# Kernel optimization log

Hardware: AMD Instinct MI355X
Metric: run time of the kernel (lower is better)

Reference implementation:

```python
import jax, jax.numpy as jnp
import numpy as np

N, D, E, H = 50000, 64, 800000, 64
LAMB = 0.8
EPS_COS = 1e-8
EPS_NORM = 1e-12


def _segment_mean(msgs, rows, n):
    # scatter_mean: sum messages per destination row, divide by in-count
    s = jax.ops.segment_sum(msgs, rows, num_segments=n)
    cnt = jax.ops.segment_sum(jnp.ones((msgs.shape[0],), msgs.dtype), rows, num_segments=n)
    return s / jnp.maximum(cnt, 1.0)[:, None]


def _l2_normalize(x):
    # F.normalize(p=2, dim=-1)
    n = jnp.linalg.norm(x, axis=-1, keepdims=True)
    return x / jnp.maximum(n, EPS_NORM)


def _base_agg(x, edges, W, b):
    row, col = edges[0], edges[1]
    agg = _segment_mean(x[col], row, x.shape[0])          # [N, D]
    out = jnp.concatenate([agg, x], axis=1) @ W + b       # [N, H]
    return _l2_normalize(out)


def _deep_agg(x1, x2, pos_edges, neg_edges, W, b):
    rp, cp = pos_edges[0], pos_edges[1]
    rn, cn = neg_edges[0], neg_edges[1]
    out1 = _segment_mean(x1[cp], rp, x1.shape[0])
    out2 = _segment_mean(x2[cn], rn, x2.shape[0])
    out = jnp.concatenate([out1, out2, x1], axis=1) @ W + b
    return _l2_normalize(out)


def _xavier(key, shape):
    fan_in, fan_out = shape
    std = np.sqrt(2.0 / (fan_in + fan_out))
    return jax.random.normal(key, shape, dtype=jnp.float32) * std


def setup_inputs() -> dict:
    key = jax.random.key(0)
    ks = jax.random.split(key, 12)
    X = jax.random.normal(ks[0], (N, D), dtype=jnp.float32)
    positive_edges = jax.random.randint(ks[1], (2, E), 0, N, dtype=jnp.int64)
    negative_edges = jax.random.randint(ks[2], (2, E), 0, N, dtype=jnp.int64)
    comm = jax.random.randint(ks[3], (N,), 0, 3, dtype=jnp.int64)
    return {
        "X": X,
        "pos_base_W": _xavier(ks[4], (2 * D, H)),
        "pos_base_b": jnp.zeros((H,), jnp.float32),
        "neg_base_W": _xavier(ks[5], (2 * D, H)),
        "neg_base_b": jnp.zeros((H,), jnp.float32),
        "pos_deep_W": _xavier(ks[6], (3 * H, H)),
        "pos_deep_b": jnp.zeros((H,), jnp.float32),
        "neg_deep_W": _xavier(ks[7], (3 * H, H)),
        "neg_deep_b": jnp.zeros((H,), jnp.float32),
        "reg_W": _xavier(ks[8], (2 * H, 3)),
        "reg_b": jnp.zeros((3,), jnp.float32),
        "positive_edges": positive_edges,
        "negative_edges": negative_edges,
        "comm": comm,
    }


def _cosine_sim(a, b):
    na = jnp.maximum(jnp.linalg.norm(a, axis=1), EPS_COS)
    nb = jnp.maximum(jnp.linalg.norm(b, axis=1), EPS_COS)
    return jnp.sum(a * b, axis=1) / (na * nb)


def reference(X, pos_base_W, pos_base_b, neg_base_W, neg_base_b,
              pos_deep_W, pos_deep_b, neg_deep_W, neg_deep_b,
              reg_W, reg_b, positive_edges, negative_edges, comm):
    # layer 0 (base aggregators) + tanh
    h_pos = jnp.tanh(_base_agg(X, positive_edges, pos_base_W, pos_base_b))
    h_neg = jnp.tanh(_base_agg(X, negative_edges, neg_base_W, neg_base_b))
    # layer 1 (deep aggregators, balance theory cross-wiring) + tanh
    h_pos2 = jnp.tanh(_deep_agg(h_pos, h_neg, positive_edges, negative_edges, pos_deep_W, pos_deep_b))
    h_neg2 = jnp.tanh(_deep_agg(h_neg, h_pos, positive_edges, negative_edges, neg_deep_W, neg_deep_b))
    z = jnp.concatenate([h_pos2, h_neg2], axis=1)          # [N, 2H]

    # nll community loss
    logits = z @ reg_W + reg_b                              # [N, 3]
    logp = jax.nn.log_softmax(logits, axis=1)
    clarify = jnp.argmax(logp, axis=1)                      # predicted classes (int)
    reg_loss = -jnp.mean(jnp.take_along_axis(logp, comm[:, None], axis=1))

    # positive similarity loss: penalize similar embeddings across predicted communities
    ip, jp = positive_edges[0], positive_edges[1]
    cos_p = _cosine_sim(z[ip], z[jp])
    sim1 = jnp.mean(jnp.where(clarify[ip] != clarify[jp], jnp.maximum(cos_p, 0.0), 0.0))

    # negative similarity loss: penalize dissimilar embeddings within predicted community
    in_, jn = negative_edges[0], negative_edges[1]
    cos_n = _cosine_sim(z[in_], z[jn])
    sim2 = jnp.mean(jnp.where(clarify[in_] == clarify[jn], -jnp.minimum(cos_n, 0.0), 0.0))

    loss = LAMB * reg_loss + (1.0 - LAMB) * (sim1 + sim2)
    return loss, z, clarify
```

## Files before the change

kernel.cpp:

```cpp
#include <hip/hip_runtime.h>
#include <hip/hip_bf16.h>
#include <math.h>

#define DFEAT 64

typedef unsigned int u32;
typedef unsigned short u16;

__device__ inline float bflo(u32 u) { return __uint_as_float(u << 16); }
__device__ inline float bfhi(u32 u) { return __uint_as_float(u & 0xffff0000u); }

__global__ void count_edges_k(const int* __restrict__ rows, int E, int* __restrict__ cnt) {
    int e = blockIdx.x * blockDim.x + threadIdx.x;
    if (e < E) atomicAdd(&cnt[rows[e]], 1);
}

__global__ __launch_bounds__(1024) void scan_k(const int* __restrict__ cnt_all, int n,
                                               int* __restrict__ offs_all, int* __restrict__ cur_all) {
    const int* cnt = cnt_all + (size_t)blockIdx.x * n;
    int* offs = offs_all + (size_t)blockIdx.x * (n + 1);
    int* cur  = cur_all  + (size_t)blockIdx.x * n;

    __shared__ int lsum[1024];
    int tid = threadIdx.x;
    int per = (n + 1023) / 1024;
    int start = tid * per;
    int s = 0;
    for (int j = 0; j < per; ++j) {
        int i = start + j;
        if (i < n) s += cnt[i];
    }
    lsum[tid] = s;
    __syncthreads();
    for (int off = 1; off < 1024; off <<= 1) {
        int v = (tid >= off) ? lsum[tid - off] : 0;
        __syncthreads();
        lsum[tid] += v;
        __syncthreads();
    }
    int running = lsum[tid] - s;
    for (int j = 0; j < per; ++j) {
        int i = start + j;
        if (i < n) {
            offs[i] = running;
            cur[i]  = running;
            running += cnt[i];
        }
    }
    if (tid == 1023) offs[n] = lsum[1023];
}

__global__ void fill_k(const int* __restrict__ rows, const int* __restrict__ cols, int E,
                       int* __restrict__ cur, int* __restrict__ col_list) {
    int e = blockIdx.x * blockDim.x + threadIdx.x;
    if (e < E) {
        int r = rows[e];
        int p = atomicAdd(&cur[r], 1);
        col_list[p] = cols[e];
    }
}

__global__ __launch_bounds__(256) void gatherX_k(
        const float* __restrict__ X,
        const int* __restrict__ offs_p, const int* __restrict__ col_p,
        const int* __restrict__ offs_n, const int* __restrict__ col_n,
        float* __restrict__ a1, float* __restrict__ a2, int n) {
    int y = blockIdx.y;
    const int* offs = y ? offs_n : offs_p;
    const int* cols = y ? col_n : col_p;
    float* o = y ? a2 : a1;
    int gid  = (blockIdx.x * blockDim.x + threadIdx.x) >> 6;
    int lane = threadIdx.x & 63;
    if (gid >= n) return;
    int beg = offs[gid], end = offs[gid + 1];
    float a = 0.f;
    int e = beg;
    for (; e + 7 < end; e += 8) {
        int c0 = cols[e],     c1 = cols[e + 1], c2 = cols[e + 2], c3 = cols[e + 3];
        int c4 = cols[e + 4], c5 = cols[e + 5], c6 = cols[e + 6], c7 = cols[e + 7];
        float v0 = X[(size_t)c0 * DFEAT + lane];
        float v1 = X[(size_t)c1 * DFEAT + lane];
        float v2 = X[(size_t)c2 * DFEAT + lane];
        float v3 = X[(size_t)c3 * DFEAT + lane];
        float v4 = X[(size_t)c4 * DFEAT + lane];
        float v5 = X[(size_t)c5 * DFEAT + lane];
        float v6 = X[(size_t)c6 * DFEAT + lane];
        float v7 = X[(size_t)c7 * DFEAT + lane];
        a += ((v0 + v1) + (v2 + v3)) + ((v4 + v5) + (v6 + v7));
    }
    for (; e + 3 < end; e += 4) {
        int c0 = cols[e], c1 = cols[e + 1], c2 = cols[e + 2], c3 = cols[e + 3];
        a += (X[(size_t)c0 * DFEAT + lane] + X[(size_t)c1 * DFEAT + lane])
           + (X[(size_t)c2 * DFEAT + lane] + X[(size_t)c3 * DFEAT + lane]);
    }
    for (; e < end; ++e) a += X[(size_t)cols[e] * DFEAT + lane];
    int deg = end - beg;
    o[(size_t)gid * DFEAT + lane] = a / (float)(deg > 1 ? deg : 1);
}

__global__ __launch_bounds__(256) void dual_gather_k(
        const float* __restrict__ hcat,
        const int* __restrict__ offs_p, const int* __restrict__ col_p,
        const int* __restrict__ offs_n, const int* __restrict__ col_n,
        float* __restrict__ a1, float* __restrict__ a2,
        float* __restrict__ z, int n) {
    int y = blockIdx.y;
    const int* offs = y ? offs_n : offs_p;
    const int* cols = y ? col_n : col_p;
    float* o1 = y ? (z + 64) : a1;  int os1 = y ? 128 : 64;
    float* o2 = y ? z        : a2;  int os2 = y ? 128 : 64;

    int gid  = (blockIdx.x * blockDim.x + threadIdx.x) >> 6;
    int lane = threadIdx.x & 63;
    if (gid >= n) return;
    int beg = offs[gid], end = offs[gid + 1];
    float sx = 0.f, sy = 0.f;
    int e = beg;
    for (; e + 7 < end; e += 8) {
        int c0 = cols[e],     c1 = cols[e + 1], c2 = cols[e + 2], c3 = cols[e + 3];
        int c4 = cols[e + 4], c5 = cols[e + 5], c6 = cols[e + 6], c7 = cols[e + 7];
        float2 v0 = *reinterpret_cast<const float2*>(hcat + (size_t)c0 * 128 + lane * 2);
        float2 v1 = *reinterpret_cast<const float2*>(hcat + (size_t)c1 * 128 + lane * 2);
        float2 v2 = *reinterpret_cast<const float2*>(hcat + (size_t)c2 * 128 + lane * 2);
        float2 v3 = *reinterpret_cast<const float2*>(hcat + (size_t)c3 * 128 + lane * 2);
        float2 v4 = *reinterpret_cast<const float2*>(hcat + (size_t)c4 * 128 + lane * 2);
        float2 v5 = *reinterpret_cast<const float2*>(hcat + (size_t)c5 * 128 + lane * 2);
        float2 v6 = *reinterpret_cast<const float2*>(hcat + (size_t)c6 * 128 + lane * 2);
        float2 v7 = *reinterpret_cast<const float2*>(hcat + (size_t)c7 * 128 + lane * 2);
        sx += ((v0.x + v1.x) + (v2.x + v3.x)) + ((v4.x + v5.x) + (v6.x + v7.x));
        sy += ((v0.y + v1.y) + (v2.y + v3.y)) + ((v4.y + v5.y) + (v6.y + v7.y));
    }
    for (; e + 3 < end; e += 4) {
        int c0 = cols[e], c1 = cols[e + 1], c2 = cols[e + 2], c3 = cols[e + 3];
        float2 v0 = *reinterpret_cast<const float2*>(hcat + (size_t)c0 * 128 + lane * 2);
        float2 v1 = *reinterpret_cast<const float2*>(hcat + (size_t)c1 * 128 + lane * 2);
        float2 v2 = *reinterpret_cast<const float2*>(hcat + (size_t)c2 * 128 + lane * 2);
        float2 v3 = *reinterpret_cast<const float2*>(hcat + (size_t)c3 * 128 + lane * 2);
        sx += (v0.x + v1.x) + (v2.x + v3.x);
        sy += (v0.y + v1.y) + (v2.y + v3.y);
    }
    for (; e < end; ++e) {
        float2 v = *reinterpret_cast<const float2*>(hcat + (size_t)cols[e] * 128 + lane * 2);
        sx += v.x; sy += v.y;
    }
    int deg = end - beg;
    float inv = 1.f / (float)(deg > 1 ? deg : 1);
    sx *= inv; sy *= inv;
    if (lane < 32) {
        o1[(size_t)gid * os1 + lane * 2]     = sx;
        o1[(size_t)gid * os1 + lane * 2 + 1] = sy;
    } else {
        o2[(size_t)gid * os2 + (lane - 32) * 2]     = sx;
        o2[(size_t)gid * os2 + (lane - 32) * 2 + 1] = sy;
    }
}

template<int K, bool HAS2>
__global__ __launch_bounds__(256) void fused_linear_k(
        const float* __restrict__ p1, int s1,
        const float* __restrict__ p2, int s2,
        const float* __restrict__ p3, int s3,
        const float* __restrict__ W, const float* __restrict__ b,
        float* __restrict__ out, int os) {
    __shared__ float Ws[K * 64];
    __shared__ float bs[64];
    __shared__ float cat[4][K];

    for (int idx = threadIdx.x; idx < K * 64; idx += 256) Ws[idx] = W[idx];
    if (threadIdx.x < 64) bs[threadIdx.x] = b[threadIdx.x];

    int wave = threadIdx.x >> 6;
    int lane = threadIdx.x & 63;
    int row  = blockIdx.x * 4 + wave;

    cat[wave][lane] = p1[(size_t)row * s1 + lane];
    if (HAS2) {
        cat[wave][64 + lane]  = p2[(size_t)row * s2 + lane];
        cat[wave][128 + lane] = p3[(size_t)row * s3 + lane];
    } else {
        cat[wave][64 + lane]  = p3[(size_t)row * s3 + lane];
    }
    __syncthreads();

    float acc = 0.f;
    #pragma unroll
    for (int k = 0; k < K; k += 4) {
        float4 cv = *reinterpret_cast<const float4*>(&cat[wave][k]);
        acc = fmaf(cv.x, Ws[(k + 0) * 64 + lane], acc);
        acc = fmaf(cv.y, Ws[(k + 1) * 64 + lane], acc);
        acc = fmaf(cv.z, Ws[(k + 2) * 64 + lane], acc);
        acc = fmaf(cv.w, Ws[(k + 3) * 64 + lane], acc);
    }
    float v = acc + bs[lane];
    float ss = v * v;
    #pragma unroll
    for (int i = 1; i < 64; i <<= 1) ss += __shfl_xor(ss, i);
    float denom = fmaxf(sqrtf(ss), 1e-12f);
    out[(size_t)row * os + lane] = tanhf(v / denom);
}

__global__ __launch_bounds__(256) void normalize_k(
        const float* __restrict__ z, u16* __restrict__ zn, int n) {
    int gid  = (blockIdx.x * blockDim.x + threadIdx.x) >> 6;
    int lane = threadIdx.x & 63;
    if (gid >= n) return;
    float v0 = z[(size_t)gid * 128 + lane * 2];
    float v1 = z[(size_t)gid * 128 + lane * 2 + 1];
    float ss = v0 * v0 + v1 * v1;
    #pragma unroll
    for (int o = 1; o < 64; o <<= 1) ss += __shfl_xor(ss, o);
    float inv = 1.f / fmaxf(sqrtf(ss), 1e-8f);
    __hip_bfloat16 b0 = __float2bfloat16(v0 * inv);
    __hip_bfloat16 b1 = __float2bfloat16(v1 * inv);
    u16 s0 = *reinterpret_cast<u16*>(&b0);
    u16 s1 = *reinterpret_cast<u16*>(&b1);
    u32 packed = (u32)s0 | ((u32)s1 << 16);
    *reinterpret_cast<u32*>(zn + (size_t)gid * 128 + lane * 2) = packed;
}

__global__ __launch_bounds__(256) void logits_k(
        const float* __restrict__ z, const float* __restrict__ Wr,
        const float* __restrict__ br, const int* __restrict__ comm,
        float* __restrict__ clar_f, int* __restrict__ clar_i,
        float* __restrict__ lp_sum, int n) {
    __shared__ float Wl[128 * 3];
    for (int idx = threadIdx.x; idx < 384; idx += blockDim.x) Wl[idx] = Wr[idx];
    __syncthreads();
    int i = blockIdx.x * blockDim.x + threadIdx.x;
    float lp = 0.f;
    if (i < n) {
        float l0 = br[0], l1 = br[1], l2 = br[2];
        const float* zr = z + (size_t)i * 128;
        #pragma unroll 4
        for (int k = 0; k < 128; k += 4) {
            float4 v = *reinterpret_cast<const float4*>(zr + k);
            float zz[4] = {v.x, v.y, v.z, v.w};
            #pragma unroll
            for (int j = 0; j < 4; ++j) {
                float zv = zz[j];
                int kk = k + j;
                l0 = fmaf(zv, Wl[3 * kk + 0], l0);
                l1 = fmaf(zv, Wl[3 * kk + 1], l1);
                l2 = fmaf(zv, Wl[3 * kk + 2], l2);
            }
        }
        int idx = 0; float mv = l0;
        if (l1 > mv) { mv = l1; idx = 1; }
        if (l2 > mv) { mv = l2; idx = 2; }
        clar_i[i] = idx;
        clar_f[i] = (float)idx;
        float lse = mv + logf(expf(l0 - mv) + expf(l1 - mv) + expf(l2 - mv));
        int c = comm[i];
        lp = (c == 0 ? l0 : (c == 1 ? l1 : l2)) - lse;
    }
    #pragma unroll
    for (int o = 1; o < 64; o <<= 1) lp += __shfl_xor(lp, o);
    __shared__ float wsum[4];
    if ((threadIdx.x & 63) == 0) wsum[threadIdx.x >> 6] = lp;
    __syncthreads();
    if (threadIdx.x == 0) atomicAdd(lp_sum, wsum[0] + wsum[1] + wsum[2] + wsum[3]);
}

__global__ __launch_bounds__(256) void sim_rows_k(
        const u16* __restrict__ zn, const int* __restrict__ clar,
        const int* __restrict__ offs_p, const int* __restrict__ col_p,
        const int* __restrict__ offs_n, const int* __restrict__ col_n,
        float* __restrict__ scal, int n) {
    int mode = blockIdx.y;
    const int* offs = mode ? offs_n : offs_p;
    const int* cols = mode ? col_n : col_p;
    int lane = threadIdx.x & 63;
    int sub  = lane & 15;
    int q    = lane >> 4;
    int wid    = blockIdx.x * 4 + (threadIdx.x >> 6);
    int nwaves = gridDim.x * 4;
    float total = 0.f;
    for (int gid = wid; gid < n; gid += nwaves) {
        uint4 ua = *reinterpret_cast<const uint4*>(zn + (size_t)gid * 128 + sub * 8);
        float a0 = bflo(ua.x), a1 = bfhi(ua.x), a2 = bflo(ua.y), a3 = bfhi(ua.y);
        float a4 = bflo(ua.z), a5 = bfhi(ua.z), a6 = bflo(ua.w), a7 = bfhi(ua.w);
        int ca = clar[gid];
        int beg = offs[gid], end = offs[gid + 1];
        #pragma unroll 2
        for (int e = beg + q; e < end; e += 4) {
            int b = cols[e];
            int cb = clar[b];
            bool sel = mode ? (cb == ca) : (cb != ca);
            if (sel) {
                uint4 ub = *reinterpret_cast<const uint4*>(zn + (size_t)b * 128 + sub * 8);
                float d;
                d = a0 * bflo(ub.x);
                d = fmaf(a1, bfhi(ub.x), d);
                d = fmaf(a2, bflo(ub.y), d);
                d = fmaf(a3, bfhi(ub.y), d);
                d = fmaf(a4, bflo(ub.z), d);
                d = fmaf(a5, bfhi(ub.z), d);
                d = fmaf(a6, bflo(ub.w), d);
                d = fmaf(a7, bfhi(ub.w), d);
                d += __shfl_xor(d, 1);
                d += __shfl_xor(d, 2);
                d += __shfl_xor(d, 4);
                d += __shfl_xor(d, 8);
                if (sub == 0) total += mode ? -fminf(d, 0.f) : fmaxf(d, 0.f);
            }
        }
    }
    #pragma unroll
    for (int o = 1; o < 64; o <<= 1) total += __shfl_xor(total, o);
    __shared__ float wsum[4];
    if ((threadIdx.x & 63) == 0) wsum[threadIdx.x >> 6] = total;
    __syncthreads();
    if (threadIdx.x == 0) atomicAdd(&scal[1 + mode], wsum[0] + wsum[1] + wsum[2] + wsum[3]);
}

__global__ void finalize_k(const float* __restrict__ scal, float* __restrict__ out,
                           int n, int E) {
    if (threadIdx.x == 0 && blockIdx.x == 0) {
        float reg_loss = -scal[0] / (float)n;
        float sim1 = scal[1] / (float)E;
        float sim2 = scal[2] / (float)E;
        out[0] = 0.8f * reg_loss + 0.2f * (sim1 + sim2);
    }
}

extern "C" void kernel_launch(void* const* d_in, const int* in_sizes, int n_in,
                              void* d_out, int out_size, void* d_ws, size_t ws_size,
                              hipStream_t stream) {
    const float* X   = (const float*)d_in[0];
    const float* pbW = (const float*)d_in[1];
    const float* pbB = (const float*)d_in[2];
    const float* nbW = (const float*)d_in[3];
    const float* nbB = (const float*)d_in[4];
    const float* pdW = (const float*)d_in[5];
    const float* pdB = (const float*)d_in[6];
    const float* ndW = (const float*)d_in[7];
    const float* ndB = (const float*)d_in[8];
    const float* rW  = (const float*)d_in[9];
    const float* rB  = (const float*)d_in[10];
    const int* pe    = (const int*)d_in[11];
    const int* ne    = (const int*)d_in[12];
    const int* comm  = (const int*)d_in[13];

    const int E = in_sizes[11] / 2;
    const int n = in_sizes[0] / DFEAT;

    float* out    = (float*)d_out;
    float* z      = out + 1;
    float* clar_f = out + 1 + (size_t)n * 128;

    char*  w   = (char*)d_ws;
    size_t big = (size_t)n * DFEAT * sizeof(float);
    float* a1    = (float*)(w);
    float* a2    = (float*)(w + big);
    float* hcat  = (float*)(w + 2 * big);
    u16*   zn    = (u16*)a1;
    char*  sm    = w + 4 * big;
    int* col_p  = (int*)sm;  sm += (size_t)E * 4;
    int* col_n  = (int*)sm;  sm += (size_t)E * 4;
    int* offs   = (int*)sm;  sm += 2 * (size_t)(n + 1) * 4;
    int* cur    = (int*)sm;  sm += 2 * (size_t)n * 4;
    int* cnt    = (int*)sm;  sm += 2 * (size_t)n * 4;
    int* clar_i = (int*)sm;  sm += (size_t)n * 4;
    float* scal = (float*)sm; sm += 64;

    int* offs_p = offs;
    int* offs_n = offs + (n + 1);
    int* cur_p  = cur;
    int* cur_n  = cur + n;
    int* cnt_p  = cnt;
    int* cnt_n  = cnt + n;

    const int* rp = pe, *cp = pe + E;
    const int* rn = ne, *cn = ne + E;

    const int egrid = (E + 255) / 256;
    const int ngrid = (n + 255) / 256;
    const int fgrid = n / 4;

    hipMemsetAsync(cnt, 0, 2 * (size_t)n * 4, stream);
    hipMemsetAsync(scal, 0, 64, stream);

    count_edges_k<<<egrid, 256, 0, stream>>>(rp, E, cnt_p);
    count_edges_k<<<egrid, 256, 0, stream>>>(rn, E, cnt_n);
    scan_k<<<2, 1024, 0, stream>>>(cnt, n, offs, cur);
    fill_k<<<egrid, 256, 0, stream>>>(rp, cp, E, cur_p, col_p);
    fill_k<<<egrid, 256, 0, stream>>>(rn, cn, E, cur_n, col_n);

    gatherX_k<<<dim3(fgrid, 2), 256, 0, stream>>>(X, offs_p, col_p, offs_n, col_n, a1, a2, n);
    fused_linear_k<128, false><<<fgrid, 256, 0, stream>>>(a1, 64, nullptr, 0, X, 64, pbW, pbB, hcat, 128);
    fused_linear_k<128, false><<<fgrid, 256, 0, stream>>>(a2, 64, nullptr, 0, X, 64, nbW, nbB, hcat + 64, 128);

    dual_gather_k<<<dim3(fgrid, 2), 256, 0, stream>>>(hcat, offs_p, col_p, offs_n, col_n, a1, a2, z, n);

    fused_linear_k<192, true><<<fgrid, 256, 0, stream>>>(a1, 64, z, 128, hcat, 128, pdW, pdB, z, 128);
    fused_linear_k<192, true><<<fgrid, 256, 0, stream>>>(a2, 64, z + 64, 128, hcat + 64, 128, ndW, ndB, z + 64, 128);

    normalize_k<<<fgrid, 256, 0, stream>>>(z, zn, n);

    logits_k<<<ngrid, 256, 0, stream>>>(z, rW, rB, comm, clar_f, clar_i, &scal[0], n);
    sim_rows_k<<<dim3(1024, 2), 256, 0, stream>>>(zn, clar_i, offs_p, col_p, offs_n, col_n, scal, n);
    finalize_k<<<1, 64, 0, stream>>>(scal, out, n, E);
}
```

Measured before the change: 928.5 us.

## Parallelize CSR prefix scan across blocks and merge pos/neg count and fill launches

Replaces the two-block serial-chunk prefix scan with a three-phase multi-block scan (per-block sums, a scan of the block sums, then a per-block local scan). This spreads the scan over about 49 blocks per edge set instead of one. The count and fill kernels for positive and negative edges are merged into single launches using blockIdx.y. The scan now takes three launches, and the block-sum scan assumes at most 64 blocks, which limits n to 65536.

After: 840.5 us. -9.5%, faster.

```diff
diff --git a/kernel.cpp b/kernel.cpp
--- a/kernel.cpp
+++ b/kernel.cpp
@@ -10,48 +10,83 @@
 __device__ inline float bflo(u32 u) { return __uint_as_float(u << 16); }
 __device__ inline float bfhi(u32 u) { return __uint_as_float(u & 0xffff0000u); }
 
-__global__ void count_edges_k(const int* __restrict__ rows, int E, int* __restrict__ cnt) {
+__global__ void count_edges_k(const int* __restrict__ rows_p, const int* __restrict__ rows_n,
+                              int E, int* __restrict__ cnt_p, int* __restrict__ cnt_n) {
+    int y = blockIdx.y;
+    const int* rows = y ? rows_n : rows_p;
+    int* cnt = y ? cnt_n : cnt_p;
     int e = blockIdx.x * blockDim.x + threadIdx.x;
     if (e < E) atomicAdd(&cnt[rows[e]], 1);
 }
 
-__global__ __launch_bounds__(1024) void scan_k(const int* __restrict__ cnt_all, int n,
-                                               int* __restrict__ offs_all, int* __restrict__ cur_all) {
-    const int* cnt = cnt_all + (size_t)blockIdx.x * n;
-    int* offs = offs_all + (size_t)blockIdx.x * (n + 1);
-    int* cur  = cur_all  + (size_t)blockIdx.x * n;
-
-    __shared__ int lsum[1024];
-    int tid = threadIdx.x;
-    int per = (n + 1023) / 1024;
-    int start = tid * per;
-    int s = 0;
-    for (int j = 0; j < per; ++j) {
-        int i = start + j;
-        if (i < n) s += cnt[i];
-    }
-    lsum[tid] = s;
-    __syncthreads();
-    for (int off = 1; off < 1024; off <<= 1) {
-        int v = (tid >= off) ? lsum[tid - off] : 0;
+__global__ __launch_bounds__(1024) void scan_partial_k(
+        const int* __restrict__ cnt_all, int n, int* __restrict__ bsum, int nb) {
+    int y = blockIdx.y;
+    const int* cnt = cnt_all + (size_t)y * n;
+    int i = blockIdx.x * 1024 + threadIdx.x;
+    int v = (i < n) ? cnt[i] : 0;
+    #pragma unroll
+    for (int o = 1; o < 64; o <<= 1) v += __shfl_xor(v, o);
+    __shared__ int sdata[16];
+    if ((threadIdx.x & 63) == 0) sdata[threadIdx.x >> 6] = v;
+    __syncthreads();
+    if (threadIdx.x < 16) {
+        int s = sdata[threadIdx.x];
+        #pragma unroll
+        for (int o = 1; o < 16; o <<= 1) s += __shfl_xor(s, o);
+        if (threadIdx.x == 0) bsum[y * nb + blockIdx.x] = s;
+    }
+}
+
+__global__ void scan_bsums_k(int* __restrict__ bsum, int nb, int n,
+                             int* __restrict__ offs_all) {
+    int y = blockIdx.x;
+    int t = threadIdx.x;
+    int orig = (t < nb) ? bsum[y * nb + t] : 0;
+    int v = orig;
+    #pragma unroll
+    for (int o = 1; o < 64; o <<= 1) {
+        int u = __shfl_up(v, o);
+        if (t >= o) v += u;
+    }
+    if (t < nb) bsum[y * nb + t] = v - orig;
+    if (t == 63) offs_all[(size_t)y * (n + 1) + n] = v;
+}
+
+__global__ __launch_bounds__(1024) void scan_final_k(
+        const int* __restrict__ cnt_all, int n, const int* __restrict__ bsum, int nb,
+        int* __restrict__ offs_all, int* __restrict__ cur_all) {
+    int y = blockIdx.y;
+    const int* cnt = cnt_all + (size_t)y * n;
+    int* offs = offs_all + (size_t)y * (n + 1);
+    int* cur  = cur_all  + (size_t)y * n;
+    int i = blockIdx.x * 1024 + threadIdx.x;
+    int v = (i < n) ? cnt[i] : 0;
+    __shared__ int ls[1024];
+    ls[threadIdx.x] = v;
+    __syncthreads();
+    for (int o = 1; o < 1024; o <<= 1) {
+        int u = (threadIdx.x >= o) ? ls[threadIdx.x - o] : 0;
         __syncthreads();
-        lsum[tid] += v;
+        ls[threadIdx.x] += u;
         __syncthreads();
     }
-    int running = lsum[tid] - s;
-    for (int j = 0; j < per; ++j) {
-        int i = start + j;
-        if (i < n) {
-            offs[i] = running;
-            cur[i]  = running;
-            running += cnt[i];
-        }
-    }
-    if (tid == 1023) offs[n] = lsum[1023];
-}
-
-__global__ void fill_k(const int* __restrict__ rows, const int* __restrict__ cols, int E,
-                       int* __restrict__ cur, int* __restrict__ col_list) {
+    if (i < n) {
+        int e = bsum[y * nb + blockIdx.x] + ls[threadIdx.x] - v;
+        offs[i] = e;
+        cur[i]  = e;
+    }
+}
+
+__global__ void fill_k(const int* __restrict__ rows_p, const int* __restrict__ cols_p,
+                       const int* __restrict__ rows_n, const int* __restrict__ cols_n,
+                       int E, int* __restrict__ cur_p, int* __restrict__ cur_n,
+                       int* __restrict__ coll_p, int* __restrict__ coll_n) {
+    int y = blockIdx.y;
+    const int* rows = y ? rows_n : rows_p;
+    const int* cols = y ? cols_n : cols_p;
+    int* cur = y ? cur_n : cur_p;
+    int* col_list = y ? coll_n : coll_p;
     int e = blockIdx.x * blockDim.x + threadIdx.x;
     if (e < E) {
         int r = rows[e];
@@ -361,6 +396,7 @@
     int* cur    = (int*)sm;  sm += 2 * (size_t)n * 4;
     int* cnt    = (int*)sm;  sm += 2 * (size_t)n * 4;
     int* clar_i = (int*)sm;  sm += (size_t)n * 4;
+    int* bsum   = (int*)sm;  sm += 2 * 64 * 4;
     float* scal = (float*)sm; sm += 64;
 
     int* offs_p = offs;
@@ -376,15 +412,16 @@
     const int egrid = (E + 255) / 256;
     const int ngrid = (n + 255) / 256;
     const int fgrid = n / 4;
+    const int nb    = (n + 1023) / 1024;
 
     hipMemsetAsync(cnt, 0, 2 * (size_t)n * 4, stream);
     hipMemsetAsync(scal, 0, 64, stream);
 
-    count_edges_k<<<egrid, 256, 0, stream>>>(rp, E, cnt_p);
-    count_edges_k<<<egrid, 256, 0, stream>>>(rn, E, cnt_n);
-    scan_k<<<2, 1024, 0, stream>>>(cnt, n, offs, cur);
-    fill_k<<<egrid, 256, 0, stream>>>(rp, cp, E, cur_p, col_p);
-    fill_k<<<egrid, 256, 0, stream>>>(rn, cn, E, cur_n, col_n);
+    count_edges_k<<<dim3(egrid, 2), 256, 0, stream>>>(rp, rn, E, cnt_p, cnt_n);
+    scan_partial_k<<<dim3(nb, 2), 1024, 0, stream>>>(cnt, n, bsum, nb);
+    scan_bsums_k<<<2, 64, 0, stream>>>(bsum, nb, n, offs);
+    scan_final_k<<<dim3(nb, 2), 1024, 0, stream>>>(cnt, n, bsum, nb, offs, cur);
+    fill_k<<<dim3(egrid, 2), 256, 0, stream>>>(rp, cp, rn, cn, E, cur_p, cur_n, col_p, col_n);
 
     gatherX_k<<<dim3(fgrid, 2), 256, 0, stream>>>(X, offs_p, col_p, offs_n, col_n, a1, a2, n);
     fused_linear_k<128, false><<<fgrid, 256, 0, stream>>>(a1, 64, nullptr, 0, X, 64, pbW, pbB, hcat, 128);
```
